# Optimization experiments

Measured on AMD Instinct MI355X. Metric: run time of the kernel, lower is better.

Reference implementation:

```python
import jax, jax.numpy as jnp
import numpy as np

N = 8192
D = 256
DENSITY = 0.02  # ~164 neighbors per node


def setup_inputs() -> dict:
    key = jax.random.key(0)
    k1, k2, k3, k4 = jax.random.split(key, 4)
    inputs = jax.random.normal(k1, (N, D), dtype=jnp.float32)
    vals = jax.random.uniform(k2, (N, N), dtype=jnp.float32, minval=0.1, maxval=1.0)
    mask = jax.random.uniform(k3, (N, N), dtype=jnp.float32) < DENSITY
    adj = jnp.where(mask, vals, 0.0)
    H_v = 0.1 * jax.random.normal(k4, (D, 1), dtype=jnp.float32)
    return {"inputs": inputs, "adj": adj, "H_v": H_v}


def reference(inputs, adj, H_v):
    # scores[j] = inputs[j] . H_v  -> sparse values v_ij = adj_ij * scores[j]
    scores = jnp.squeeze(inputs @ H_v, -1)            # [N]
    mask = adj != 0.0                                  # nonzero pattern of SparseTensor
    logits = adj * scores[None, :]                     # [N, N]
    neg = jnp.asarray(jnp.finfo(logits.dtype).min, logits.dtype)
    logits = jnp.where(mask, logits, neg)
    # sparse softmax: normalize only over nonzero entries per row
    m = jnp.max(logits, axis=1, keepdims=True)
    e = jnp.where(mask, jnp.exp(logits - m), 0.0)
    s = jnp.sum(e, axis=1, keepdims=True)
    weights = e / jnp.where(s > 0, s, 1.0)             # empty rows -> all-zero weights
    # sparse_tensor_dense_matmul(weights, inputs)
    return weights @ inputs                            # [N, D]
```

## Files before the change

kernel.cpp:

```cpp
#include <hip/hip_runtime.h>

#define NN 8192
#define DD 256
#define RCAP 1024

typedef float v4f __attribute__((ext_vector_type(4)));
typedef unsigned short u16x4 __attribute__((ext_vector_type(4)));
typedef unsigned short u16x8 __attribute__((ext_vector_type(8)));

__device__ __forceinline__ unsigned short f2bf_rne(float x) {
    unsigned u = __float_as_uint(x);
    u += 0x7fffu + ((u >> 16) & 1u);
    return (unsigned short)(u >> 16);
}

template <bool WRITE_IB>
__global__ __launch_bounds__(256) void prep_kernel(const float* __restrict__ inputs,
                                                   const float* __restrict__ Hv,
                                                   float* __restrict__ scores,
                                                   unsigned short* __restrict__ ib) {
    int wave = threadIdx.x >> 6;
    int lane = threadIdx.x & 63;
    int row  = blockIdx.x * 4 + wave;
    float4 v = ((const float4*)(inputs + (size_t)row * DD))[lane];
    if (WRITE_IB) {
        u16x4 u;
        u.x = f2bf_rne(v.x); u.y = f2bf_rne(v.y); u.z = f2bf_rne(v.z); u.w = f2bf_rne(v.w);
        ((u16x4*)(ib + (size_t)row * DD))[lane] = u;
    }
    float4 h = ((const float4*)Hv)[lane];
    float s = v.x * h.x + v.y * h.y + v.z * h.z + v.w * h.w;
    #pragma unroll
    for (int off = 32; off > 0; off >>= 1) s += __shfl_down(s, off, 64);
    if (lane == 0) scores[row] = s;
}

__device__ __forceinline__ void batch8x2(const unsigned short* __restrict__ ib,
                                         int jl, int el, int m, int sel, int lane8,
                                         float4& accL, float4& accH, float& ssum) {
    int js[8]; float es[8];
#pragma unroll
    for (int u = 0; u < 8; ++u) {
        js[u] = __builtin_amdgcn_readlane(jl, m + u);
        es[u] = __uint_as_float(__builtin_amdgcn_readlane(el, m + u));
    }
    u16x8 g[4];
#pragma unroll
    for (int p = 0; p < 4; ++p) {
        int j = sel ? js[2 * p + 1] : js[2 * p];
        g[p] = *(const u16x8*)(ib + (size_t)j * DD + lane8);
    }
#pragma unroll
    for (int p = 0; p < 4; ++p) {
        float e = sel ? es[2 * p + 1] : es[2 * p];
        float4 lo, hi;
        lo.x = __uint_as_float((unsigned)g[p][0] << 16);
        lo.y = __uint_as_float((unsigned)g[p][1] << 16);
        lo.z = __uint_as_float((unsigned)g[p][2] << 16);
        lo.w = __uint_as_float((unsigned)g[p][3] << 16);
        hi.x = __uint_as_float((unsigned)g[p][4] << 16);
        hi.y = __uint_as_float((unsigned)g[p][5] << 16);
        hi.z = __uint_as_float((unsigned)g[p][6] << 16);
        hi.w = __uint_as_float((unsigned)g[p][7] << 16);
        accL.x += e * lo.x; accL.y += e * lo.y; accL.z += e * lo.z; accL.w += e * lo.w;
        accH.x += e * hi.x; accH.y += e * hi.y; accH.z += e * hi.z; accH.w += e * hi.w;
        ssum += e;
    }
}

__device__ __forceinline__ void gather_range(const float2* __restrict__ s_je, int b, int ke,
                                             const unsigned short* __restrict__ ib, int lane,
                                             float4& accL, float4& accH, float& ssum) {
    const int sel   = lane >> 5;
    const int lane8 = (lane & 31) * 8;
    while (b < ke) {
        int n = ke - b; n = n > 64 ? 64 : n;
        float2 je = s_je[b + (lane < n ? lane : 0)];
        if (lane >= n) je.y = 0.f;
        int jl = __float_as_int(je.x);
        int el = __float_as_int(je.y);
        int n8 = (n + 7) & ~7;
        for (int m = 0; m < n8; m += 8)
            batch8x2(ib, jl, el, m, sel, lane8, accL, accH, ssum);
        b += n;
    }
}

__global__ __launch_bounds__(256) void fused_kernel(const float* __restrict__ adj,
                                                    const float* __restrict__ scores,
                                                    const unsigned short* __restrict__ ib,
                                                    float* __restrict__ out) {
    __shared__ float2 s_je[RCAP];
    __shared__ float  s_red[8 * DD];
    __shared__ float  s_ss[8];
    __shared__ int    s_wsum[4];
    __shared__ int    s_cnt;

    const int tid  = threadIdx.x;
    const int lane = tid & 63;
    const int wave = tid >> 6;
    const int row  = blockIdx.x;

    const v4f* p = (const v4f*)(adj + (size_t)row * NN);
    v4f a[8];
#pragma unroll
    for (int c = 0; c < 8; ++c) a[c] = __builtin_nontemporal_load(&p[c * 256 + tid]);

    int nz = 0;
#pragma unroll
    for (int c = 0; c < 8; ++c)
        nz += (a[c].x != 0.f) + (a[c].y != 0.f) + (a[c].z != 0.f) + (a[c].w != 0.f);
    int pre = nz;
#pragma unroll
    for (int off = 1; off < 64; off <<= 1) {
        int t = __shfl_up(pre, off, 64);
        if (lane >= off) pre += t;
    }
    if (lane == 63) s_wsum[wave] = pre;
    __syncthreads();
    int base = 0, total = 0;
#pragma unroll
    for (int w = 0; w < 4; ++w) {
        int t = s_wsum[w];
        if (w < wave) base += t;
        total += t;
    }

    float4 accL = make_float4(0.f, 0.f, 0.f, 0.f), accH = accL;
    float ssum = 0.f;

    if (total <= RCAP) {
        int off = base + pre - nz;
#pragma unroll
        for (int c = 0; c < 8; ++c) {
            int j0 = c * 1024 + tid * 4;
            float v;
            v = a[c].x; if (v != 0.f) { s_je[off] = make_float2(__int_as_float(j0 + 0), __expf(v * scores[j0 + 0])); off++; }
            v = a[c].y; if (v != 0.f) { s_je[off] = make_float2(__int_as_float(j0 + 1), __expf(v * scores[j0 + 1])); off++; }
            v = a[c].z; if (v != 0.f) { s_je[off] = make_float2(__int_as_float(j0 + 2), __expf(v * scores[j0 + 2])); off++; }
            v = a[c].w; if (v != 0.f) { s_je[off] = make_float2(__int_as_float(j0 + 3), __expf(v * scores[j0 + 3])); off++; }
        }
        __syncthreads();
        gather_range(s_je, wave * total / 4, (wave + 1) * total / 4, ib, lane, accL, accH, ssum);
    } else {
        for (int c = 0; c < 8; ++c) {
            if (tid == 0) s_cnt = 0;
            __syncthreads();
            int j0 = c * 1024 + tid * 4;
            float v;
            v = a[c].x; if (v != 0.f) { int k = atomicAdd(&s_cnt, 1); s_je[k] = make_float2(__int_as_float(j0 + 0), __expf(v * scores[j0 + 0])); }
            v = a[c].y; if (v != 0.f) { int k = atomicAdd(&s_cnt, 1); s_je[k] = make_float2(__int_as_float(j0 + 1), __expf(v * scores[j0 + 1])); }
            v = a[c].z; if (v != 0.f) { int k = atomicAdd(&s_cnt, 1); s_je[k] = make_float2(__int_as_float(j0 + 2), __expf(v * scores[j0 + 2])); }
            v = a[c].w; if (v != 0.f) { int k = atomicAdd(&s_cnt, 1); s_je[k] = make_float2(__int_as_float(j0 + 3), __expf(v * scores[j0 + 3])); }
            __syncthreads();
            int tc = s_cnt;
            gather_range(s_je, wave * tc / 4, (wave + 1) * tc / 4, ib, lane, accL, accH, ssum);
            __syncthreads();
        }
    }

    const int half = wave * 2 + (lane >> 5);
    const int l8   = (lane & 31) * 8;
    if ((lane & 31) == 0) s_ss[half] = ssum;
    *(float4*)&s_red[half * DD + l8]     = accL;
    *(float4*)&s_red[half * DD + l8 + 4] = accH;
    __syncthreads();
    float tot = 0.f;
#pragma unroll
    for (int i = 0; i < 8; ++i) tot += s_ss[i];
    float r = 0.f;
#pragma unroll
    for (int i = 0; i < 8; ++i) r += s_red[i * DD + tid];
    out[(size_t)row * DD + tid] = (tot > 0.f) ? r / tot : 0.f;
}

__global__ __launch_bounds__(256) void attn_fallback(const float* __restrict__ adj,
                                                     const float* __restrict__ inputs,
                                                     const float* __restrict__ scores,
                                                     float* __restrict__ out) {
    __shared__ int   s_j[1024];
    __shared__ float s_e[1024];
    __shared__ int   s_cnt;
    const int row = blockIdx.x;
    const int tid = threadIdx.x;
    const float* arow = adj + (size_t)row * NN;
    float acc = 0.f, ssum = 0.f;
    for (int base = 0; base < NN; base += 1024) {
        if (tid == 0) s_cnt = 0;
        __syncthreads();
        float4 a = ((const float4*)(arow + base))[tid];
        int j0 = base + tid * 4;
        if (a.x != 0.f) { int k = atomicAdd(&s_cnt, 1); s_j[k] = j0 + 0; s_e[k] = __expf(a.x * scores[j0 + 0]); }
        if (a.y != 0.f) { int k = atomicAdd(&s_cnt, 1); s_j[k] = j0 + 1; s_e[k] = __expf(a.y * scores[j0 + 1]); }
        if (a.z != 0.f) { int k = atomicAdd(&s_cnt, 1); s_j[k] = j0 + 2; s_e[k] = __expf(a.z * scores[j0 + 2]); }
        if (a.w != 0.f) { int k = atomicAdd(&s_cnt, 1); s_j[k] = j0 + 3; s_e[k] = __expf(a.w * scores[j0 + 3]); }
        __syncthreads();
        int c = s_cnt;
        for (int k = 0; k < c; ++k) {
            float e = s_e[k];
            acc  += e * inputs[(size_t)s_j[k] * DD + tid];
            ssum += e;
        }
        __syncthreads();
    }
    out[(size_t)row * DD + tid] = (ssum > 0.f) ? acc / ssum : 0.f;
}

extern "C" void kernel_launch(void* const* d_in, const int* in_sizes, int n_in,
                              void* d_out, int out_size, void* d_ws, size_t ws_size,
                              hipStream_t stream) {
    const float* inputs = (const float*)d_in[0];
    const float* adj    = (const float*)d_in[1];
    const float* Hv     = (const float*)d_in[2];
    float* out = (float*)d_out;

    char* ws = (char*)d_ws;
    float*          scores = (float*)ws;
    unsigned short* ib     = (unsigned short*)(ws + 32768);

    const size_t need = 32768 + (size_t)NN * DD * 2;

    if (ws_size >= need) {
        prep_kernel<true><<<NN / 4, 256, 0, stream>>>(inputs, Hv, scores, ib);
        fused_kernel<<<NN, 256, 0, stream>>>(adj, scores, ib, out);
    } else {
        prep_kernel<false><<<NN / 4, 256, 0, stream>>>(inputs, Hv, scores, nullptr);
        attn_fallback<<<NN, 256, 0, stream>>>(adj, inputs, scores, out);
    }
}
```

Baseline: 409.1 us.

## Give each wave its own column slice and LDS segment, dropping block barriers

Each wave now loads a contiguous 2048-column slice of the adjacency row and compacts its nonzeros into a private LDS segment using a wave-local prefix scan. This removes the cross-wave scan, the shared counter and the block-wide __syncthreads calls. The gather loop now reads index/weight pairs straight from LDS instead of broadcasting them with readlane, and pads segments to a multiple of eight with zero entries. Load balance now depends on how nonzeros fall across the column quarters rather than an even split of the total. The overflow path (more than 256 nonzeros per wave) is handled per chunk with wave-local scans.

```diff
diff --git a/kernel.cpp b/kernel.cpp
--- a/kernel.cpp
+++ b/kernel.cpp
@@ -2,7 +2,9 @@
 
 #define NN 8192
 #define DD 256
-#define RCAP 1024
+#define WCOLS 2048
+#define WCAP 256
+#define WSEG 264
 
 typedef float v4f __attribute__((ext_vector_type(4)));
 typedef unsigned short u16x4 __attribute__((ext_vector_type(4)));
@@ -35,54 +37,31 @@
     if (lane == 0) scores[row] = s;
 }
 
-__device__ __forceinline__ void batch8x2(const unsigned short* __restrict__ ib,
-                                         int jl, int el, int m, int sel, int lane8,
-                                         float4& accL, float4& accH, float& ssum) {
-    int js[8]; float es[8];
-#pragma unroll
-    for (int u = 0; u < 8; ++u) {
-        js[u] = __builtin_amdgcn_readlane(jl, m + u);
-        es[u] = __uint_as_float(__builtin_amdgcn_readlane(el, m + u));
-    }
-    u16x8 g[4];
-#pragma unroll
-    for (int p = 0; p < 4; ++p) {
-        int j = sel ? js[2 * p + 1] : js[2 * p];
-        g[p] = *(const u16x8*)(ib + (size_t)j * DD + lane8);
-    }
-#pragma unroll
-    for (int p = 0; p < 4; ++p) {
-        float e = sel ? es[2 * p + 1] : es[2 * p];
-        float4 lo, hi;
-        lo.x = __uint_as_float((unsigned)g[p][0] << 16);
-        lo.y = __uint_as_float((unsigned)g[p][1] << 16);
-        lo.z = __uint_as_float((unsigned)g[p][2] << 16);
-        lo.w = __uint_as_float((unsigned)g[p][3] << 16);
-        hi.x = __uint_as_float((unsigned)g[p][4] << 16);
-        hi.y = __uint_as_float((unsigned)g[p][5] << 16);
-        hi.z = __uint_as_float((unsigned)g[p][6] << 16);
-        hi.w = __uint_as_float((unsigned)g[p][7] << 16);
-        accL.x += e * lo.x; accL.y += e * lo.y; accL.z += e * lo.z; accL.w += e * lo.w;
-        accH.x += e * hi.x; accH.y += e * hi.y; accH.z += e * hi.z; accH.w += e * hi.w;
-        ssum += e;
-    }
-}
-
-__device__ __forceinline__ void gather_range(const float2* __restrict__ s_je, int b, int ke,
-                                             const unsigned short* __restrict__ ib, int lane,
-                                             float4& accL, float4& accH, float& ssum) {
-    const int sel   = lane >> 5;
-    const int lane8 = (lane & 31) * 8;
-    while (b < ke) {
-        int n = ke - b; n = n > 64 ? 64 : n;
-        float2 je = s_je[b + (lane < n ? lane : 0)];
-        if (lane >= n) je.y = 0.f;
-        int jl = __float_as_int(je.x);
-        int el = __float_as_int(je.y);
-        int n8 = (n + 7) & ~7;
-        for (int m = 0; m < n8; m += 8)
-            batch8x2(ib, jl, el, m, sel, lane8, accL, accH, ssum);
-        b += n;
+__device__ __forceinline__ void gather_seg(const float2* __restrict__ s_seg, int n8,
+                                           const unsigned short* __restrict__ ib,
+                                           int sel, int lane8,
+                                           float4& accL, float4& accH, float& ssum) {
+    for (int m = 0; m < n8; m += 8) {
+        float2 je[4];
+#pragma unroll
+        for (int p = 0; p < 4; ++p) je[p] = s_seg[m + 2 * p + sel];
+        u16x8 g[4];
+#pragma unroll
+        for (int p = 0; p < 4; ++p)
+            g[p] = *(const u16x8*)(ib + (size_t)__float_as_int(je[p].x) * DD + lane8);
+#pragma unroll
+        for (int p = 0; p < 4; ++p) {
+            float e = je[p].y;
+            accL.x += e * __uint_as_float((unsigned)g[p][0] << 16);
+            accL.y += e * __uint_as_float((unsigned)g[p][1] << 16);
+            accL.z += e * __uint_as_float((unsigned)g[p][2] << 16);
+            accL.w += e * __uint_as_float((unsigned)g[p][3] << 16);
+            accH.x += e * __uint_as_float((unsigned)g[p][4] << 16);
+            accH.y += e * __uint_as_float((unsigned)g[p][5] << 16);
+            accH.z += e * __uint_as_float((unsigned)g[p][6] << 16);
+            accH.w += e * __uint_as_float((unsigned)g[p][7] << 16);
+            ssum += e;
+        }
     }
 }
 
@@ -90,21 +69,23 @@
                                                     const float* __restrict__ scores,
                                                     const unsigned short* __restrict__ ib,
                                                     float* __restrict__ out) {
-    __shared__ float2 s_je[RCAP];
+    __shared__ float2 s_je[4][WSEG];
     __shared__ float  s_red[8 * DD];
     __shared__ float  s_ss[8];
-    __shared__ int    s_wsum[4];
-    __shared__ int    s_cnt;
-
-    const int tid  = threadIdx.x;
-    const int lane = tid & 63;
-    const int wave = tid >> 6;
-    const int row  = blockIdx.x;
-
-    const v4f* p = (const v4f*)(adj + (size_t)row * NN);
+
+    const int tid   = threadIdx.x;
+    const int lane  = tid & 63;
+    const int wave  = tid >> 6;
+    const int row   = blockIdx.x;
+    const int sel   = lane >> 5;
+    const int lane8 = (lane & 31) * 8;
+    const int colbase = wave * WCOLS + lane * 4;
+
+    const float* arow = adj + (size_t)row * NN;
     v4f a[8];
 #pragma unroll
-    for (int c = 0; c < 8; ++c) a[c] = __builtin_nontemporal_load(&p[c * 256 + tid]);
+    for (int c = 0; c < 8; ++c)
+        a[c] = __builtin_nontemporal_load(((const v4f*)(arow + wave * WCOLS + c * 256)) + lane);
 
     int nz = 0;
 #pragma unroll
@@ -116,54 +97,59 @@
         int t = __shfl_up(pre, off, 64);
         if (lane >= off) pre += t;
     }
-    if (lane == 63) s_wsum[wave] = pre;
-    __syncthreads();
-    int base = 0, total = 0;
-#pragma unroll
-    for (int w = 0; w < 4; ++w) {
-        int t = s_wsum[w];
-        if (w < wave) base += t;
-        total += t;
-    }
+    const int total = __shfl(pre, 63, 64);
 
     float4 accL = make_float4(0.f, 0.f, 0.f, 0.f), accH = accL;
     float ssum = 0.f;
-
-    if (total <= RCAP) {
-        int off = base + pre - nz;
+    float2* seg = s_je[wave];
+
+    if (total <= WCAP) {
+        int off = pre - nz;
 #pragma unroll
         for (int c = 0; c < 8; ++c) {
-            int j0 = c * 1024 + tid * 4;
+            int j0 = colbase + c * 256;
             float v;
-            v = a[c].x; if (v != 0.f) { s_je[off] = make_float2(__int_as_float(j0 + 0), __expf(v * scores[j0 + 0])); off++; }
-            v = a[c].y; if (v != 0.f) { s_je[off] = make_float2(__int_as_float(j0 + 1), __expf(v * scores[j0 + 1])); off++; }
-            v = a[c].z; if (v != 0.f) { s_je[off] = make_float2(__int_as_float(j0 + 2), __expf(v * scores[j0 + 2])); off++; }
-            v = a[c].w; if (v != 0.f) { s_je[off] = make_float2(__int_as_float(j0 + 3), __expf(v * scores[j0 + 3])); off++; }
-        }
-        __syncthreads();
-        gather_range(s_je, wave * total / 4, (wave + 1) * total / 4, ib, lane, accL, accH, ssum);
+            v = a[c].x; if (v != 0.f) { seg[off] = make_float2(__int_as_float(j0 + 0), __expf(v * scores[j0 + 0])); off++; }
+            v = a[c].y; if (v != 0.f) { seg[off] = make_float2(__int_as_float(j0 + 1), __expf(v * scores[j0 + 1])); off++; }
+            v = a[c].z; if (v != 0.f) { seg[off] = make_float2(__int_as_float(j0 + 2), __expf(v * scores[j0 + 2])); off++; }
+            v = a[c].w; if (v != 0.f) { seg[off] = make_float2(__int_as_float(j0 + 3), __expf(v * scores[j0 + 3])); off++; }
+        }
+        const int n8 = (total + 7) & ~7;
+        if (lane < n8 - total) seg[total + lane] = make_float2(0.f, 0.f);
+        asm volatile("s_waitcnt lgkmcnt(0)" ::: "memory");
+        __builtin_amdgcn_sched_barrier(0);
+        gather_seg(seg, n8, ib, sel, lane8, accL, accH, ssum);
     } else {
         for (int c = 0; c < 8; ++c) {
-            if (tid == 0) s_cnt = 0;
-            __syncthreads();
-            int j0 = c * 1024 + tid * 4;
+            int cn = (a[c].x != 0.f) + (a[c].y != 0.f) + (a[c].z != 0.f) + (a[c].w != 0.f);
+            int cpre = cn;
+#pragma unroll
+            for (int off = 1; off < 64; off <<= 1) {
+                int t = __shfl_up(cpre, off, 64);
+                if (lane >= off) cpre += t;
+            }
+            int ctotal = __shfl(cpre, 63, 64);
+            int off = cpre - cn;
+            int j0 = colbase + c * 256;
             float v;
-            v = a[c].x; if (v != 0.f) { int k = atomicAdd(&s_cnt, 1); s_je[k] = make_float2(__int_as_float(j0 + 0), __expf(v * scores[j0 + 0])); }
-            v = a[c].y; if (v != 0.f) { int k = atomicAdd(&s_cnt, 1); s_je[k] = make_float2(__int_as_float(j0 + 1), __expf(v * scores[j0 + 1])); }
-            v = a[c].z; if (v != 0.f) { int k = atomicAdd(&s_cnt, 1); s_je[k] = make_float2(__int_as_float(j0 + 2), __expf(v * scores[j0 + 2])); }
-            v = a[c].w; if (v != 0.f) { int k = atomicAdd(&s_cnt, 1); s_je[k] = make_float2(__int_as_float(j0 + 3), __expf(v * scores[j0 + 3])); }
-            __syncthreads();
-            int tc = s_cnt;
-            gather_range(s_je, wave * tc / 4, (wave + 1) * tc / 4, ib, lane, accL, accH, ssum);
-            __syncthreads();
-        }
-    }
-
-    const int half = wave * 2 + (lane >> 5);
-    const int l8   = (lane & 31) * 8;
+            v = a[c].x; if (v != 0.f) { seg[off] = make_float2(__int_as_float(j0 + 0), __expf(v * scores[j0 + 0])); off++; }
+            v = a[c].y; if (v != 0.f) { seg[off] = make_float2(__int_as_float(j0 + 1), __expf(v * scores[j0 + 1])); off++; }
+            v = a[c].z; if (v != 0.f) { seg[off] = make_float2(__int_as_float(j0 + 2), __expf(v * scores[j0 + 2])); off++; }
+            v = a[c].w; if (v != 0.f) { seg[off] = make_float2(__int_as_float(j0 + 3), __expf(v * scores[j0 + 3])); off++; }
+            int cn8 = (ctotal + 7) & ~7;
+            if (lane < cn8 - ctotal) seg[ctotal + lane] = make_float2(0.f, 0.f);
+            asm volatile("s_waitcnt lgkmcnt(0)" ::: "memory");
+            __builtin_amdgcn_sched_barrier(0);
+            gather_seg(seg, cn8, ib, sel, lane8, accL, accH, ssum);
+            asm volatile("s_waitcnt lgkmcnt(0)" ::: "memory");
+            __builtin_amdgcn_sched_barrier(0);
+        }
+    }
+
+    const int half = wave * 2 + sel;
     if ((lane & 31) == 0) s_ss[half] = ssum;
-    *(float4*)&s_red[half * DD + l8]     = accL;
-    *(float4*)&s_red[half * DD + l8 + 4] = accH;
+    *(float4*)&s_red[half * DD + lane8]     = accL;
+    *(float4*)&s_red[half * DD + lane8 + 4] = accH;
     __syncthreads();
     float tot = 0.f;
 #pragma unroll
```

New measurement: 405.8 us. About the same (-0.8%).
